# Kernel tuning notes

Measured on AMD Instinct MI355X. Metric: run time of the kernel, lower is better.

The kernel has to match this reference:

```python
import jax, jax.numpy as jnp
import numpy as np
from jax import lax

HID = 768          # hidden_dim / embedding_dim
IN = 64            # input_dim = max_seq_length // num_heads
SEQ = 512          # max_seq_length
GROUPS = IN        # conv groups
BLUR_K = 5
BLUR_SIGMA = 1.0


def _gauss1d(k, sigma):
    half = (k - 1) * 0.5
    x = np.linspace(-half, half, k)
    pdf = np.exp(-0.5 * (x / sigma) ** 2)
    return pdf / pdf.sum()


def setup_inputs() -> dict:
    key = jax.random.key(0)
    ks = jax.random.split(key, 8)
    s = 0.02
    return {
        "inputs": jax.random.normal(ks[0], (16, SEQ, HID), jnp.float32),
        # Conv1d(768, 768, k=3, groups=64): weight [out_ch, in_ch/groups, k]
        "conv_w": jax.random.normal(ks[1], (HID, HID // GROUPS, 3), jnp.float32) * s,
        "conv_b": jnp.zeros((HID,), jnp.float32),
        "ln_g": jnp.ones((IN,), jnp.float32),
        "ln_b": jnp.zeros((IN,), jnp.float32),
        # function_info: Linear(64, 64), torch weight convention [out, in]
        "fi_w": jax.random.normal(ks[2], (IN, IN), jnp.float32) * s,
        "fi_b": jnp.zeros((IN,), jnp.float32),
        # block_info: Linear(64, 1)
        "bi_w": jax.random.normal(ks[3], (1, IN), jnp.float32) * s,
        "bi_b": jnp.zeros((1,), jnp.float32),
    }


def _forward(inputs, conv_w, conv_b, ln_g, ln_b, fi_w, fi_b, bi_w, bi_b):
    x = inputs.reshape(-1, HID, IN)  # [Bn, 768, 64] (raw row-major view, as torch .view)
    q = k = v = m = x

    # q: grouped Conv1d + residual, GELU, LayerNorm over last dim (64)
    qc = lax.conv_general_dilated(
        q, conv_w, window_strides=(1,), padding=[(1, 1)],
        feature_group_count=GROUPS, dimension_numbers=("NCH", "OIH", "NCH"))
    qc = qc + conv_b[None, :, None]
    q = jax.nn.gelu(qc + q, approximate=False)
    mu = jnp.mean(q, axis=-1, keepdims=True)
    var = jnp.mean(jnp.square(q - mu), axis=-1, keepdims=True)
    q = (q - mu) * lax.rsqrt(var + 1e-5) * ln_g + ln_b

    # v: Linear(64,64) + GELU
    v = jax.nn.gelu(v @ fi_w.T + fi_b, approximate=False)

    # k: dropout (eval -> identity), softmax over dim=-2 (channel axis), GELU
    k = jax.nn.gelu(jax.nn.softmax(k, axis=-2), approximate=False)

    # m: GaussianBlur(5, sigma fixed 1.0) over (H=768, W=64) with reflect pad, then Linear(64,1)
    g = _gauss1d(BLUR_K, BLUR_SIGMA)
    kern = jnp.asarray(np.outer(g, g), m.dtype)[None, None]  # [1,1,5,5]
    p = BLUR_K // 2
    mp = jnp.pad(m[:, None], ((0, 0), (0, 0), (p, p), (p, p)), mode="reflect")
    m = lax.conv_general_dilated(
        mp, kern, (1, 1), "VALID", dimension_numbers=("NCHW", "OIHW", "NCHW"))[:, 0]
    m = m @ bi_w.T + bi_b                        # [Bn, 768, 1]
    mask = jnp.broadcast_to(m, (m.shape[0], HID, HID))  # expand to [Bn,768,768]

    # SDPA: scale = 1/sqrt(E) with E = q.shape[-1] = 64; additive float mask
    scores = jnp.einsum("bce,bde->bcd", q, k) * (1.0 / np.sqrt(IN)) + mask
    attn = jax.nn.softmax(scores, axis=-1)
    out = jnp.einsum("bcd,bde->bce", attn, v)    # [Bn, 768, 64]
    return out.reshape(-1, SEQ, HID)


def reference(inputs, conv_w, conv_b, ln_g, ln_b, fi_w, fi_b, bi_w, bi_b):
    return _forward(inputs, conv_w, conv_b, ln_g, ln_b, fi_w, fi_b, bi_w, bi_b)
```

## Files before the change

### kernel.cpp

```cpp
#include <hip/hip_runtime.h>
#include <hip/hip_bf16.h>
#include <math.h>

#define NB 128
#define NC 768
#define NE 64
#define IPG 12

typedef __hip_bfloat16 bf16;
typedef __bf16 bf16v8 __attribute__((ext_vector_type(8)));
typedef __bf16 bf16v4 __attribute__((ext_vector_type(4)));
typedef __bf16 bf16v2 __attribute__((ext_vector_type(2)));
typedef float f32x4 __attribute__((ext_vector_type(4)));
typedef unsigned int u32;
typedef u32 u32x4 __attribute__((ext_vector_type(4)));

__device__ __forceinline__ float gelu_exact(float x) {
    float ax = fabsf(x);
    float t = __builtin_amdgcn_rcpf(fmaf(0.2316419f, ax, 1.0f));
    float poly = t * fmaf(t, fmaf(t, fmaf(t, fmaf(t, 1.330274429f,
                  -1.821255978f), 1.781477937f), -0.356563782f), 0.319381530f);
    float pdf = 0.3989422804f * __expf(-0.5f * ax * ax);
    float c = fmaf(-pdf, poly, 1.0f);
    float cdf = (x >= 0.f) ? c : 1.0f - c;
    return x * cdf;
}

#define MFMA16(a, b, c) __builtin_amdgcn_mfma_f32_16x16x32_bf16(a, b, c, 0, 0, 0)

__device__ __forceinline__ void gload_lds16(const void* g, void* l) {
    __builtin_amdgcn_global_load_lds(
        (const __attribute__((address_space(1))) void*)g,
        (__attribute__((address_space(3))) void*)l, 16, 0, 0);
}

__global__ __launch_bounds__(256) void k_prod(
    const float* __restrict__ x, const float* __restrict__ cw,
    const float* __restrict__ cb, const float* __restrict__ lg,
    const float* __restrict__ lb, const float* __restrict__ fw,
    const float* __restrict__ fb, bf16* __restrict__ qo,
    float* __restrict__ sp, bf16* __restrict__ vt2)
{
    int chunk = blockIdx.x;
    int b = blockIdx.y;
    int w = threadIdx.x >> 6, h = threadIdx.x & 63;
    const float* xb = x + (size_t)b * NC * NE;
    float gam = lg[h], bet = lb[h];

    float es = 0.f;
    for (int gi = 0; gi < 2; ++gi) {
        int g = __builtin_amdgcn_readfirstlane(chunk * 8 + gi * 4 + w);
        const float* xg = xb + (size_t)g * IPG * NE;

        float xi[IPG], xm[IPG], xp[IPG];
        #pragma unroll
        for (int i = 0; i < IPG; ++i) {
            xi[i] = xg[i * NE + h];
            float up = __shfl_up(xi[i], 1);
            float dn = __shfl_down(xi[i], 1);
            xm[i] = h ? up : 0.f;
            xp[i] = (h < 63) ? dn : 0.f;
            es += __expf(xi[i]);
        }
        const float* wg = cw + (size_t)g * IPG * 36;
        for (int o = 0; o < IPG; ++o) {
            const float* wo = wg + o * 36;
            float acc = cb[g * IPG + o];
            #pragma unroll
            for (int i = 0; i < IPG; ++i)
                acc = fmaf(xm[i], wo[i*3], fmaf(xi[i], wo[i*3+1], fmaf(xp[i], wo[i*3+2], acc)));
            float gl = gelu_exact(acc + xi[o]);
            float s1 = gl, s2 = gl * gl;
            #pragma unroll
            for (int off = 32; off; off >>= 1) {
                s1 += __shfl_xor(s1, off);
                s2 += __shfl_xor(s2, off);
            }
            float mu  = s1 * (1.f / 64.f);
            float var = s2 * (1.f / 64.f) - mu * mu;
            float qn = (gl - mu) * rsqrtf(var + 1e-5f) * gam + bet;
            qo[((size_t)b * NC + g * IPG + o) * NE + h] = __float2bfloat16(qn * 0.125f);
        }
    }

    __shared__ float red[4][64];
    red[w][h] = es;
    __syncthreads();
    if (w == 0)
        sp[(size_t)(b * 8 + chunk) * 64 + h] =
            red[0][h] + red[1][h] + red[2][h] + red[3][h];

    int l = threadIdx.x & 63;
    int lr = l & 15, lc = (l >> 4) * 8;

    bf16v8 bfr[4][2];
    float fbias[4];
    #pragma unroll
    for (int nt = 0; nt < 4; ++nt) {
        #pragma unroll
        for (int kt = 0; kt < 2; ++kt) {
            const float* p = fw + (nt*16 + lr) * 64 + kt*32 + lc;
            bf16v8 t;
            #pragma unroll
            for (int j = 0; j < 8; ++j) t[j] = (__bf16)p[j];
            bfr[nt][kt] = t;
        }
        fbias[nt] = fb[nt*16 + lr];
    }

    for (int t = w; t < 6; t += 4) {
        int trow = chunk * 96 + t * 16;
        const float* pa = xb + (size_t)(trow + lr) * NE;
        bf16v8 a0, a1;
        #pragma unroll
        for (int j = 0; j < 8; ++j) a0[j] = (__bf16)pa[lc + j];
        #pragma unroll
        for (int j = 0; j < 8; ++j) a1[j] = (__bf16)pa[32 + lc + j];

        int c0 = trow + (l >> 4) * 4;
        int ktile = c0 >> 5, kc = c0 & 31;
        #pragma unroll
        for (int nt = 0; nt < 4; ++nt) {
            f32x4 acc = {fbias[nt], fbias[nt], fbias[nt], fbias[nt]};
            acc = MFMA16(a0, bfr[nt][0], acc);
            acc = MFMA16(a1, bfr[nt][1], acc);
            bf16v4 pk;
            #pragma unroll
            for (int r = 0; r < 4; ++r) pk[r] = (__bf16)gelu_exact(acc[r]);
            *(bf16v4*)&vt2[(((size_t)b * 24 + ktile) * 64 + nt*16 + lr) * 32 + kc] = pk;
        }
    }
}

__global__ __launch_bounds__(256) void k_kbuild(
    const float* __restrict__ x, const float* __restrict__ sp,
    bf16* __restrict__ ko)
{
    int chunk = blockIdx.x, b = blockIdx.y;
    int tid = threadIdx.x, w = tid >> 6, l = tid & 63;
    int lr = l & 15, lc = (l >> 4) * 8;
    int rowb = chunk * 64 + w * 16;

    __shared__ float sts[64];
    if (tid < 64) {
        float s = 0.f;
        #pragma unroll
        for (int p = 0; p < 8; ++p) s += sp[(size_t)(b * 8 + p) * 64 + tid];
        sts[tid] = 1.f / s;
    }
    __syncthreads();

    float isA[8], isB[8];
    #pragma unroll
    for (int j = 0; j < 8; ++j) { isA[j] = sts[lc + j]; isB[j] = sts[32 + lc + j]; }

    const float* pa = x + ((size_t)b * NC + rowb + lr) * NE;
    bf16v8 kv0, kv1;
    #pragma unroll
    for (int j = 0; j < 8; ++j) kv0[j] = (__bf16)gelu_exact(__expf(pa[lc + j]) * isA[j]);
    #pragma unroll
    for (int j = 0; j < 8; ++j) kv1[j] = (__bf16)gelu_exact(__expf(pa[32 + lc + j]) * isB[j]);
    bf16* kp = ko + ((size_t)b * NC + rowb + lr) * NE + lc;
    *(bf16v8*)kp = kv0;
    *(bf16v8*)(kp + 32) = kv1;
}

__device__ __forceinline__ bf16v8 softmax_exch(f32x4 s0, f32x4 s1, float& rsum,
                                               int srcA, int srcB, int hq) {
    float p0 = __expf(s0[0]), p1 = __expf(s0[1]), p2 = __expf(s0[2]), p3 = __expf(s0[3]);
    float p4 = __expf(s1[0]), p5 = __expf(s1[1]), p6 = __expf(s1[2]), p7 = __expf(s1[3]);
    rsum += ((p0 + p1) + (p2 + p3)) + ((p4 + p5) + (p6 + p7));
    bf16v2 t0; t0[0] = (__bf16)p0; t0[1] = (__bf16)p1;
    bf16v2 t1; t1[0] = (__bf16)p2; t1[1] = (__bf16)p3;
    bf16v2 t2; t2[0] = (__bf16)p4; t2[1] = (__bf16)p5;
    bf16v2 t3; t3[0] = (__bf16)p6; t3[1] = (__bf16)p7;
    u32 w0 = __builtin_bit_cast(u32, t0), w1 = __builtin_bit_cast(u32, t1);
    u32 w2 = __builtin_bit_cast(u32, t2), w3 = __builtin_bit_cast(u32, t3);
    u32 c0A = (u32)__shfl((int)w0, srcA), c1A = (u32)__shfl((int)w1, srcA);
    u32 c2A = (u32)__shfl((int)w2, srcA), c3A = (u32)__shfl((int)w3, srcA);
    u32 c0B = (u32)__shfl((int)w0, srcB), c1B = (u32)__shfl((int)w1, srcB);
    u32 c2B = (u32)__shfl((int)w2, srcB), c3B = (u32)__shfl((int)w3, srcB);
    u32x4 pau = { hq ? c2A : c0A, hq ? c3A : c1A,
                  hq ? c2B : c0B, hq ? c3B : c1B };
    return __builtin_bit_cast(bf16v8, pau);
}

__global__ __launch_bounds__(256, 3) void k_attn(const bf16* __restrict__ qb,
                                                 const bf16* __restrict__ kb,
                                                 const bf16* __restrict__ vt2,
                                                 float* __restrict__ out) {
    __shared__ __align__(16) __bf16 ldsK[2][4096];
    __shared__ __align__(16) __bf16 ldsV[2][4096];

    int bid = blockIdx.x;
    int swz = (bid & 7) * 96 + (bid >> 3);
    int b = swz / 6, qt = swz - b * 6;
    int w = threadIdx.x >> 6, l = threadIdx.x & 63;
    int q0 = qt * 128 + w * 32;
    int lr = l & 15, hi = l >> 4;
    int hq = hi >> 1;
    int srcA = lr + ((hi & 1) << 5);
    int srcB = srcA + 16;

    int krow_ = w * 8 + (l >> 3);
    int kc16_ = (l & 7) ^ (l >> 3);
    const char* kgbase = (const char*)(kb + (size_t)b * NC * NE)
                       + krow_ * 128 + kc16_ * 16;
    int ve_   = w * 16 + (l >> 2);
    int vc16_ = (l & 3) ^ ((l >> 3) & 3);
    const char* vgbase = (const char*)vt2 + (size_t)b * 24 * 4096
                       + ve_ * 64 + vc16_ * 16;

    int krd0 = lr * 64 + ((hi ^ (lr & 7)) << 3);
    int krd1 = lr * 64 + (((4 + hi) ^ (lr & 7)) << 3);
    int vsel = (lr >> 1) & 3;
    int vrd  = lr * 32 + ((hi ^ vsel) << 3);

    const bf16* qp = qb + ((size_t)b * NC + q0 + lr) * NE + hi * 8;
    bf16v8 qf00 = *(const bf16v8*)qp;
    bf16v8 qf01 = *(const bf16v8*)(qp + 32);
    bf16v8 qf10 = *(const bf16v8*)(qp + 16 * NE);
    bf16v8 qf11 = *(const bf16v8*)(qp + 16 * NE + 32);

    f32x4 o00 = {0,0,0,0}, o01 = {0,0,0,0}, o02 = {0,0,0,0}, o03 = {0,0,0,0};
    f32x4 o10 = {0,0,0,0}, o11 = {0,0,0,0}, o12 = {0,0,0,0}, o13 = {0,0,0,0};
    float rsum0 = 0.f, rsum1 = 0.f;

    gload_lds16(kgbase,        &ldsK[0][w * 512]);
    gload_lds16(kgbase + 4096, &ldsK[0][2048 + w * 512]);
    gload_lds16(vgbase,        &ldsV[0][w * 512]);
    gload_lds16(vgbase + 4096, &ldsV[0][2048 + w * 512]);
    __syncthreads();

    int cur = 0;
    for (int ph = 0; ph < 12; ++ph) {
        if (ph < 11) {
            const char* kg = kgbase + (size_t)(2 * ph + 2) * 4096;
            gload_lds16(kg,        &ldsK[cur ^ 1][w * 512]);
            gload_lds16(kg + 4096, &ldsK[cur ^ 1][2048 + w * 512]);
            const char* vg = vgbase + (size_t)(2 * ph + 2) * 4096;
            gload_lds16(vg,        &ldsV[cur ^ 1][w * 512]);
            gload_lds16(vg + 4096, &ldsV[cur ^ 1][2048 + w * 512]);
        }

        #pragma unroll
        for (int sub = 0; sub < 2; ++sub) {
            const __bf16* Kc = &ldsK[cur][sub * 2048];
            const __bf16* Vc = &ldsV[cur][sub * 2048];
            bf16v8 ka0 = *(const bf16v8*)&Kc[krd0];
            bf16v8 ka1 = *(const bf16v8*)&Kc[krd1];
            bf16v8 ka2 = *(const bf16v8*)&Kc[krd0 + 1024];
            bf16v8 ka3 = *(const bf16v8*)&Kc[krd1 + 1024];
            bf16v8 v0  = *(const bf16v8*)&Vc[vrd];
            bf16v8 v1  = *(const bf16v8*)&Vc[vrd + 512];
            bf16v8 v2  = *(const bf16v8*)&Vc[vrd + 1024];
            bf16v8 v3  = *(const bf16v8*)&Vc[vrd + 1536];

            __builtin_amdgcn_s_setprio(1);
            f32x4 s00 = {0,0,0,0}, s01 = {0,0,0,0};
            s00 = MFMA16(ka0, qf00, s00);
            s00 = MFMA16(ka1, qf01, s00);
            s01 = MFMA16(ka2, qf00, s01);
            s01 = MFMA16(ka3, qf01, s01);
            f32x4 s10 = {0,0,0,0}, s11 = {0,0,0,0};
            s10 = MFMA16(ka0, qf10, s10);
            s10 = MFMA16(ka1, qf11, s10);
            s11 = MFMA16(ka2, qf10, s11);
            s11 = MFMA16(ka3, qf11, s11);
            __builtin_amdgcn_s_setprio(0);

            bf16v8 pa0 = softmax_exch(s00, s01, rsum0, srcA, srcB, hq);
            bf16v8 pa1 = softmax_exch(s10, s11, rsum1, srcA, srcB, hq);

            __builtin_amdgcn_s_setprio(1);
            o00 = MFMA16(pa0, v0, o00);
            o01 = MFMA16(pa0, v1, o01);
            o02 = MFMA16(pa0, v2, o02);
            o03 = MFMA16(pa0, v3, o03);
            o10 = MFMA16(pa1, v0, o10);
            o11 = MFMA16(pa1, v1, o11);
            o12 = MFMA16(pa1, v2, o12);
            o13 = MFMA16(pa1, v3, o13);
            __builtin_amdgcn_s_setprio(0);
        }

        __syncthreads();
        cur ^= 1;
    }

    rsum0 += __shfl_xor(rsum0, 16);
    rsum0 += __shfl_xor(rsum0, 32);
    rsum1 += __shfl_xor(rsum1, 16);
    rsum1 += __shfl_xor(rsum1, 32);
    float inv0 = 1.f / rsum0, inv1 = 1.f / rsum1;

    int qrow0 = q0 + hi * 4;
    #pragma unroll
    for (int r = 0; r < 4; ++r) {
        float iq = __shfl(inv0, hi * 4 + r);
        float* op = out + ((size_t)b * NC + qrow0 + r) * NE + lr;
        op[0]  = o00[r] * iq;
        op[16] = o01[r] * iq;
        op[32] = o02[r] * iq;
        op[48] = o03[r] * iq;
    }
    int qrow1 = q0 + 16 + hi * 4;
    #pragma unroll
    for (int r = 0; r < 4; ++r) {
        float iq = __shfl(inv1, hi * 4 + r);
        float* op = out + ((size_t)b * NC + qrow1 + r) * NE + lr;
        op[0]  = o10[r] * iq;
        op[16] = o11[r] * iq;
        op[32] = o12[r] * iq;
        op[48] = o13[r] * iq;
    }
}

extern "C" void kernel_launch(void* const* d_in, const int* in_sizes, int n_in,
                              void* d_out, int out_size, void* d_ws, size_t ws_size,
                              hipStream_t stream) {
    (void)in_sizes; (void)n_in; (void)out_size; (void)ws_size;
    const float* x      = (const float*)d_in[0];
    const float* conv_w = (const float*)d_in[1];
    const float* conv_b = (const float*)d_in[2];
    const float* ln_g   = (const float*)d_in[3];
    const float* ln_b   = (const float*)d_in[4];
    const float* fi_w   = (const float*)d_in[5];
    const float* fi_b   = (const float*)d_in[6];

    bf16* qbuf = (bf16*)d_ws;
    bf16* kbuf = qbuf + (size_t)NB * NC * NE;
    bf16* vt2  = kbuf + (size_t)NB * NC * NE;
    float* stats = (float*)(vt2 + (size_t)NB * NC * NE);
    float* out = (float*)d_out;

    k_prod<<<dim3(8, NB), 256, 0, stream>>>(x, conv_w, conv_b, ln_g, ln_b,
                                            fi_w, fi_b, qbuf, stats, vt2);
    k_kbuild<<<dim3(12, NB), 256, 0, stream>>>(x, stats, kbuf);
    k_attn<<<dim3(768), 256, 0, stream>>>(qbuf, kbuf, vt2, out);
}
```

Before: 79.64 us.

## Split producer kernel into separate conv and V-projection blocks for more parallelism

The producer kernel previously ran 1024 blocks, each doing two conv groups per wave plus a V-projection tile loop. It now launches 3584 blocks: 2048 handle one conv group per wave (with partial exp-sums written per 16-chunk), and 1536 handle the MFMA V-projection, one 16-row tile per wave. The goal is better occupancy and load balance across CUs and less serial work per block. In exchange, stats partials double and the V blocks each reload the fi_w fragments.

```diff
diff --git a/kernel.cpp b/kernel.cpp
--- a/kernel.cpp
+++ b/kernel.cpp
@@ -34,35 +34,47 @@
         (__attribute__((address_space(3))) void*)l, 16, 0, 0);
 }
 
-__global__ __launch_bounds__(256) void k_prod(
+__global__ __launch_bounds__(256) void k_prod2(
     const float* __restrict__ x, const float* __restrict__ cw,
     const float* __restrict__ cb, const float* __restrict__ lg,
     const float* __restrict__ lb, const float* __restrict__ fw,
     const float* __restrict__ fb, bf16* __restrict__ qo,
     float* __restrict__ sp, bf16* __restrict__ vt2)
 {
-    int chunk = blockIdx.x;
-    int b = blockIdx.y;
-    int w = threadIdx.x >> 6, h = threadIdx.x & 63;
-    const float* xb = x + (size_t)b * NC * NE;
-    float gam = lg[h], bet = lb[h];
-
-    float es = 0.f;
-    for (int gi = 0; gi < 2; ++gi) {
-        int g = __builtin_amdgcn_readfirstlane(chunk * 8 + gi * 4 + w);
-        const float* xg = xb + (size_t)g * IPG * NE;
+    __shared__ float red[4][64];
+    int bid = blockIdx.x;
+    int tid = threadIdx.x, w = tid >> 6, l = tid & 63;
+
+    if (bid < 2048) {
+        int b = bid >> 4;
+        int chunk = bid & 15;
+        int g = __builtin_amdgcn_readfirstlane(chunk * 4 + w);
+        int h = l;
+        const float* xb = x + ((size_t)b * NC + g * IPG) * NE;
 
         float xi[IPG], xm[IPG], xp[IPG];
         #pragma unroll
         for (int i = 0; i < IPG; ++i) {
-            xi[i] = xg[i * NE + h];
+            xi[i] = xb[i * NE + h];
             float up = __shfl_up(xi[i], 1);
             float dn = __shfl_down(xi[i], 1);
             xm[i] = h ? up : 0.f;
             xp[i] = (h < 63) ? dn : 0.f;
-            es += __expf(xi[i]);
-        }
+        }
+
+        float es = 0.f;
+        #pragma unroll
+        for (int i = 0; i < IPG; ++i) es += __expf(xi[i]);
+        red[w][h] = es;
+        __syncthreads();
+        if (w == 0) {
+            float s = red[0][h] + red[1][h] + red[2][h] + red[3][h];
+            sp[(size_t)(b * 16 + chunk) * 64 + h] = s;
+        }
+
+        float gam = lg[h], bet = lb[h];
         const float* wg = cw + (size_t)g * IPG * 36;
+
         for (int o = 0; o < IPG; ++o) {
             const float* wo = wg + o * 36;
             float acc = cb[g * IPG + o];
@@ -81,43 +93,37 @@
             float qn = (gl - mu) * rsqrtf(var + 1e-5f) * gam + bet;
             qo[((size_t)b * NC + g * IPG + o) * NE + h] = __float2bfloat16(qn * 0.125f);
         }
-    }
-
-    __shared__ float red[4][64];
-    red[w][h] = es;
-    __syncthreads();
-    if (w == 0)
-        sp[(size_t)(b * 8 + chunk) * 64 + h] =
-            red[0][h] + red[1][h] + red[2][h] + red[3][h];
-
-    int l = threadIdx.x & 63;
-    int lr = l & 15, lc = (l >> 4) * 8;
-
-    bf16v8 bfr[4][2];
-    float fbias[4];
-    #pragma unroll
-    for (int nt = 0; nt < 4; ++nt) {
-        #pragma unroll
-        for (int kt = 0; kt < 2; ++kt) {
-            const float* p = fw + (nt*16 + lr) * 64 + kt*32 + lc;
-            bf16v8 t;
+    } else {
+        int vid = bid - 2048;
+        int chunk = vid % 12;
+        int b = vid / 12;
+        int lr = l & 15, lc = (l >> 4) * 8;
+        int rowb = chunk * 64 + w * 16;
+        const float* xb = x + (size_t)b * NC * NE;
+
+        bf16v8 bfr[4][2];
+        float fbias[4];
+        #pragma unroll
+        for (int nt = 0; nt < 4; ++nt) {
             #pragma unroll
-            for (int j = 0; j < 8; ++j) t[j] = (__bf16)p[j];
-            bfr[nt][kt] = t;
-        }
-        fbias[nt] = fb[nt*16 + lr];
-    }
-
-    for (int t = w; t < 6; t += 4) {
-        int trow = chunk * 96 + t * 16;
-        const float* pa = xb + (size_t)(trow + lr) * NE;
+            for (int kt = 0; kt < 2; ++kt) {
+                const float* p = fw + (nt*16 + lr) * 64 + kt*32 + lc;
+                bf16v8 t;
+                #pragma unroll
+                for (int j = 0; j < 8; ++j) t[j] = (__bf16)p[j];
+                bfr[nt][kt] = t;
+            }
+            fbias[nt] = fb[nt*16 + lr];
+        }
+
+        const float* pa = xb + (size_t)(rowb + lr) * NE;
         bf16v8 a0, a1;
         #pragma unroll
         for (int j = 0; j < 8; ++j) a0[j] = (__bf16)pa[lc + j];
         #pragma unroll
         for (int j = 0; j < 8; ++j) a1[j] = (__bf16)pa[32 + lc + j];
 
-        int c0 = trow + (l >> 4) * 4;
+        int c0 = rowb + (l >> 4) * 4;
         int ktile = c0 >> 5, kc = c0 & 31;
         #pragma unroll
         for (int nt = 0; nt < 4; ++nt) {
@@ -145,7 +151,7 @@
     if (tid < 64) {
         float s = 0.f;
         #pragma unroll
-        for (int p = 0; p < 8; ++p) s += sp[(size_t)(b * 8 + p) * 64 + tid];
+        for (int p = 0; p < 16; ++p) s += sp[(size_t)(b * 16 + p) * 64 + tid];
         sts[tid] = 1.f / s;
     }
     __syncthreads();
@@ -334,8 +340,9 @@
     float* stats = (float*)(vt2 + (size_t)NB * NC * NE);
     float* out = (float*)d_out;
 
-    k_prod<<<dim3(8, NB), 256, 0, stream>>>(x, conv_w, conv_b, ln_g, ln_b,
-                                            fi_w, fi_b, qbuf, stats, vt2);
+    k_prod2<<<dim3(2048 + 1536), 256, 0, stream>>>(x, conv_w, conv_b, ln_g,
+                                                   ln_b, fi_w, fi_b, qbuf,
+                                                   stats, vt2);
     k_kbuild<<<dim3(12, NB), 256, 0, stream>>>(x, stats, kbuf);
     k_attn<<<dim3(768), 256, 0, stream>>>(qbuf, kbuf, vt2, out);
 }
```

New measurement: 79.29 us. About the same (-0.4%).
